# Kernel tuning notes

Hardware: AMD Instinct MI355X
Metric: run time of the kernel (lower is better)

## Reference

```python
import jax, jax.numpy as jnp
import numpy as np

B, N, G, OUT = 2, 250000, 64, 64          # batches, points per batch, grid per axis, out feat dim
NS = B * G * G * G                          # total voxel segments
EPS = 1e-5


def _bn(x, g, b, m, v):
    # BatchNorm1d in eval mode: affine with running stats
    return (x - m) * (g * jax.lax.rsqrt(v + EPS)) + b


def setup_inputs() -> dict:
    key = jax.random.key(0)
    ks = jax.random.split(key, 32)
    d = {}
    d["pt_fea"] = jax.random.normal(ks[0], (B, N, 3), jnp.float32)
    d["pt_ind"] = jax.random.randint(ks[1], (B, N, 3), 0, G)
    i = 2
    for j, dm in enumerate([3, 64, 128, 256]):
        d[f"bn{j}_g"] = jax.random.uniform(ks[i], (dm,), jnp.float32, 0.5, 1.5); i += 1
        d[f"bn{j}_b"] = jax.random.normal(ks[i], (dm,), jnp.float32) * 0.1; i += 1
        d[f"bn{j}_m"] = jax.random.normal(ks[i], (dm,), jnp.float32) * 0.1; i += 1
        d[f"bn{j}_v"] = jax.random.uniform(ks[i], (dm,), jnp.float32, 0.5, 1.5); i += 1
    for j, (fi, fo) in enumerate([(3, 64), (64, 128), (128, 256), (256, OUT)]):
        d[f"W{j}"] = jax.random.normal(ks[i], (fi, fo), jnp.float32) / np.float32(np.sqrt(fi)); i += 1
        d[f"b{j}"] = jnp.zeros((fo,), jnp.float32); i += 1
    return d


def reference(pt_fea, pt_ind,
              bn0_g, bn0_b, bn0_m, bn0_v,
              bn1_g, bn1_b, bn1_m, bn1_v,
              bn2_g, bn2_b, bn2_m, bn2_v,
              bn3_g, bn3_b, bn3_m, bn3_v,
              W0, b0, W1, b1, W2, b2, W3, b3):
    P = B * N
    x = pt_fea.reshape(P, 3)
    ind = pt_ind.reshape(P, 3)                       # (x, y, z) -> reorder to (z, y, x)
    b_idx = jnp.repeat(jnp.arange(B, dtype=ind.dtype), N)
    # linearized (batch, z, y, x) voxel id; hwl reorder as in original
    seg = ((b_idx * G + ind[:, 2]) * G + ind[:, 1]) * G + ind[:, 0]

    # PPmodel: BN -> Lin -> BN -> ReLU -> Lin -> BN -> ReLU -> Lin -> BN -> ReLU -> Lin
    h = _bn(x, bn0_g, bn0_b, bn0_m, bn0_v)
    h = jax.nn.relu(_bn(h @ W0 + b0, bn1_g, bn1_b, bn1_m, bn1_v))
    h = jax.nn.relu(_bn(h @ W1 + b1, bn2_g, bn2_b, bn2_m, bn2_v))
    h = jax.nn.relu(_bn(h @ W2 + b2, bn3_g, bn3_b, bn3_m, bn3_v))
    h = h @ W3 + b3                                   # [P, OUT]

    pooled = jax.ops.segment_max(h, seg, num_segments=NS)        # [NS, OUT]
    cnt = jax.ops.segment_sum(jnp.ones((P,), jnp.float32), seg, num_segments=NS)
    # torch_scatter.scatter_max leaves empty rows at 0
    voxel_features = jnp.where(cnt[:, None] > 0, pooled, 0.0)
    return voxel_features
```

## Files before the change

### kernel.cpp

```cpp
#include <hip/hip_runtime.h>


using bf16x8 = __attribute__((ext_vector_type(8))) short;
using f32x4  = __attribute__((ext_vector_type(4))) float;

constexpr int Bc = 2, Nc = 250000, Pc = 500000, Gc = 64, NSc = 524288;
constexpr float EPSV = 1e-5f;
constexpr int W0E = 0;
constexpr int W1E = 4096;
constexpr int W2E = 20480;
constexpr int W3E = 86016;
constexpr int CB_BYTES = 2048;

#define MFMA __builtin_amdgcn_mfma_f32_16x16x32_bf16

__device__ __forceinline__ bf16x8 mk8(unsigned a, unsigned b, unsigned c, unsigned d) {
  union { unsigned u[4]; bf16x8 v; } x;
  x.u[0] = a; x.u[1] = b; x.u[2] = c; x.u[3] = d;
  return x.v;
}

__device__ __forceinline__ void gload16(const unsigned short* src, unsigned short* dst_lds) {
  __builtin_amdgcn_global_load_lds(
      (const __attribute__((address_space(1))) unsigned int*)(const void*)src,
      (__attribute__((address_space(3))) unsigned int*)(void*)dst_lds, 16, 0, 0);
}

__device__ __forceinline__ unsigned fenc(float f) {
  unsigned b = __float_as_uint(f);
  return (b & 0x80000000u) ? ~b : (b | 0x80000000u);
}
__device__ __forceinline__ unsigned fdec(unsigned u) {
  if (u == 0u) return 0u;
  return (u & 0x80000000u) ? (u & 0x7fffffffu) : ~u;
}

__global__ void init_out_kernel(uint4* __restrict__ p, int n4) {
  int i = blockIdx.x * blockDim.x + threadIdx.x;
  const int st = gridDim.x * blockDim.x;
  const uint4 z = make_uint4(0u, 0u, 0u, 0u);
  for (; i < n4; i += st) p[i] = z;
}

__global__ void decode_out_kernel(uint4* __restrict__ p, int n4) {
  int i = blockIdx.x * blockDim.x + threadIdx.x;
  const int st = gridDim.x * blockDim.x;
  for (; i < n4; i += st) {
    uint4 u = p[i];
    u.x = fdec(u.x); u.y = fdec(u.y); u.z = fdec(u.z); u.w = fdec(u.w);
    p[i] = u;
  }
}

__global__ void prep_kernel(
    const float* __restrict__ G0, const float* __restrict__ B0, const float* __restrict__ M0, const float* __restrict__ V0,
    const float* __restrict__ G1, const float* __restrict__ B1, const float* __restrict__ M1, const float* __restrict__ V1,
    const float* __restrict__ G2, const float* __restrict__ B2, const float* __restrict__ M2, const float* __restrict__ V2,
    const float* __restrict__ G3, const float* __restrict__ B3, const float* __restrict__ M3, const float* __restrict__ V3,
    const float* __restrict__ W0, const float* __restrict__ bb0,
    const float* __restrict__ W1, const float* __restrict__ bb1,
    const float* __restrict__ W2, const float* __restrict__ bb2,
    const float* __restrict__ W3, const float* __restrict__ bb3,
    float* __restrict__ cb, unsigned short* __restrict__ wsu)
{
  const int i = blockIdx.x * 256 + threadIdx.x;
  if (i < 59392) {
    const int u = i >> 9, pos = i & 511;
    const int lane = pos >> 3, j = pos & 7;
    const int row16 = lane & 15, kin = (lane >> 4) * 8 + j;
    float v; int dstbase;
    if (u < 4) {
      const int mt = u, fo = mt * 16 + row16, k = kin;
      const float t1 = G1[fo] * rsqrtf(V1[fo] + EPSV);
      v = (k < 3) ? (G0[k] * rsqrtf(V0[k] + EPSV)) * W0[k * 64 + fo] * t1 : 0.f;
      dstbase = W0E + u * 1024;
    } else if (u < 20) {
      const int q = u - 4, mt = q >> 1, kt = q & 1;
      const int fo = mt * 16 + row16, k = kt * 32 + kin;
      v = W1[k * 128 + fo] * (G2[fo] * rsqrtf(V2[fo] + EPSV));
      dstbase = W1E + q * 1024;
    } else if (u < 84) {
      const int q = u - 20, mt = q >> 2, kt = q & 3;
      const int fo = mt * 16 + row16, k = kt * 32 + kin;
      v = W2[k * 256 + fo] * (G3[fo] * rsqrtf(V3[fo] + EPSV));
      dstbase = W2E + q * 1024;
    } else {
      const int q = u - 84, kt = q >> 2, nt = q & 3;
      const int k = kt * 32 + kin, fo = nt * 16 + row16;
      v = W3[k * 64 + fo];
      dstbase = W3E + q * 1024;
    }
    const unsigned uh = __float_as_uint(v) & 0xffff0000u;
    const float lo = v - __uint_as_float(uh);
    wsu[dstbase + pos]       = (unsigned short)(uh >> 16);
    wsu[dstbase + 512 + pos] = (unsigned short)(__float_as_uint(lo) >> 16);
  } else if (i < 59904) {
    const int f = i - 59392;
    if (f < 64) {
      const int fo = f;
      const float t1 = G1[fo] * rsqrtf(V1[fo] + EPSV);
      float s = 0.f;
      for (int c = 0; c < 3; ++c) {
        const float t0 = G0[c] * rsqrtf(V0[c] + EPSV);
        s += (B0[c] - M0[c] * t0) * W0[c * 64 + fo];
      }
      cb[fo] = (bb0[fo] + s - M1[fo]) * t1 + B1[fo];
    } else if (f < 192) {
      const int fo = f - 64;
      const float t2 = G2[fo] * rsqrtf(V2[fo] + EPSV);
      cb[64 + fo] = (bb1[fo] - M2[fo]) * t2 + B2[fo];
    } else if (f < 448) {
      const int fo = f - 192;
      const float t3 = G3[fo] * rsqrtf(V3[fo] + EPSV);
      cb[192 + fo] = (bb2[fo] - M3[fo]) * t3 + B3[fo];
    } else {
      const int fo = f - 448;
      cb[448 + fo] = bb3[fo];
    }
  }
}

struct PKp { unsigned h0, h1, l0, l1; };

__device__ __forceinline__ PKp epi_relu(f32x4 d, f32x4 cbv) {
  const float e0 = fmaxf(d[0] + cbv[0], 0.f), e1 = fmaxf(d[1] + cbv[1], 0.f);
  const float e2 = fmaxf(d[2] + cbv[2], 0.f), e3 = fmaxf(d[3] + cbv[3], 0.f);
  const unsigned u0 = __float_as_uint(e0) & 0xffff0000u, u1 = __float_as_uint(e1) & 0xffff0000u;
  const unsigned u2 = __float_as_uint(e2) & 0xffff0000u, u3 = __float_as_uint(e3) & 0xffff0000u;
  PKp r;
  r.h0 = (u0 >> 16) | u1;
  r.h1 = (u2 >> 16) | u3;
  const float f0 = e0 - __uint_as_float(u0), f1 = e1 - __uint_as_float(u1);
  const float f2 = e2 - __uint_as_float(u2), f3 = e3 - __uint_as_float(u3);
  r.l0 = (__float_as_uint(f0) >> 16) | (__float_as_uint(f1) & 0xffff0000u);
  r.l1 = (__float_as_uint(f2) >> 16) | (__float_as_uint(f3) & 0xffff0000u);
  return r;
}

__device__ __forceinline__ void trans2(const PKp& A, const PKp& B, int lane,
                                       bf16x8& fh, bf16x8& fl) {
  const int idx0 = ((lane & 15) << 2) | (((lane >> 4) & 1) << 7);
  const int idx1 = idx0 + 64;
  const bool hi = lane >= 32;
  unsigned v0, v1, v2, v3;
  { unsigned a = __builtin_amdgcn_ds_bpermute(idx0, (int)A.h0), b = __builtin_amdgcn_ds_bpermute(idx0, (int)B.h0); v0 = hi ? b : a; }
  { unsigned a = __builtin_amdgcn_ds_bpermute(idx0, (int)A.h1), b = __builtin_amdgcn_ds_bpermute(idx0, (int)B.h1); v1 = hi ? b : a; }
  { unsigned a = __builtin_amdgcn_ds_bpermute(idx1, (int)A.h0), b = __builtin_amdgcn_ds_bpermute(idx1, (int)B.h0); v2 = hi ? b : a; }
  { unsigned a = __builtin_amdgcn_ds_bpermute(idx1, (int)A.h1), b = __builtin_amdgcn_ds_bpermute(idx1, (int)B.h1); v3 = hi ? b : a; }
  fh = mk8(v0, v1, v2, v3);
  { unsigned a = __builtin_amdgcn_ds_bpermute(idx0, (int)A.l0), b = __builtin_amdgcn_ds_bpermute(idx0, (int)B.l0); v0 = hi ? b : a; }
  { unsigned a = __builtin_amdgcn_ds_bpermute(idx0, (int)A.l1), b = __builtin_amdgcn_ds_bpermute(idx0, (int)B.l1); v1 = hi ? b : a; }
  { unsigned a = __builtin_amdgcn_ds_bpermute(idx1, (int)A.l0), b = __builtin_amdgcn_ds_bpermute(idx1, (int)B.l0); v2 = hi ? b : a; }
  { unsigned a = __builtin_amdgcn_ds_bpermute(idx1, (int)A.l1), b = __builtin_amdgcn_ds_bpermute(idx1, (int)B.l1); v3 = hi ? b : a; }
  fl = mk8(v0, v1, v2, v3);
}

__global__ __launch_bounds__(512, 2)
void mlp_mfma(const float* __restrict__ pt_fea, const int* __restrict__ pt_ind,
              const unsigned short* __restrict__ wsu, const float* __restrict__ cb,
              unsigned* __restrict__ out)
{
  __shared__ __align__(16) unsigned short lds[49152];

  const int tid = threadIdx.x, lane = tid & 63, wv = tid >> 6;
  const int g = lane >> 4, c16 = lane & 15;
  const int pw = (blockIdx.x * 8 + wv) * 32;

  #pragma unroll
  for (int c = 0; c < 4; ++c) {
    const int ch = wv * 4 + c;
    gload16(wsu + W1E + ch * 512 + lane * 8, &lds[ch * 512]);
  }
  #pragma unroll
  for (int c = 0; c < 8; ++c) {
    const int ch = wv * 8 + c;
    gload16(wsu + W2E + ch * 512 + lane * 8, &lds[16384 + ch * 512]);
  }

  bf16x8 b0h[2], b0l[2];
  #pragma unroll
  for (int nt = 0; nt < 2; ++nt) {
    const int p = pw + nt * 16 + c16;
    float x = 0.f, y = 0.f, z = 0.f;
    if (p < Pc) { x = pt_fea[p * 3]; y = pt_fea[p * 3 + 1]; z = pt_fea[p * 3 + 2]; }
    const unsigned ux = __float_as_uint(x) & 0xffff0000u;
    const unsigned uy = __float_as_uint(y) & 0xffff0000u;
    const unsigned uz = __float_as_uint(z) & 0xffff0000u;
    const float lx = x - __uint_as_float(ux), ly = y - __uint_as_float(uy), lz = z - __uint_as_float(uz);
    const unsigned ph0 = (ux >> 16) | uy, ph1 = (uz >> 16);
    const unsigned pl0 = (__float_as_uint(lx) >> 16) | (__float_as_uint(ly) & 0xffff0000u);
    const unsigned pl1 = (__float_as_uint(lz) >> 16);
    const bool g0ok = (g == 0);
    b0h[nt] = mk8(g0ok ? ph0 : 0u, g0ok ? ph1 : 0u, 0u, 0u);
    b0l[nt] = mk8(g0ok ? pl0 : 0u, g0ok ? pl1 : 0u, 0u, 0u);
  }

  bf16x8 B1h[2][2], B1l[2][2];
  #pragma unroll
  for (int K = 0; K < 2; ++K) {
    PKp pk[2][2];
    #pragma unroll
    for (int e = 0; e < 2; ++e) {
      const int mt = 2 * K + e;
      const bf16x8 wh = *(const bf16x8*)(wsu + W0E + mt * 1024 + lane * 8);
      const bf16x8 wl = *(const bf16x8*)(wsu + W0E + mt * 1024 + 512 + lane * 8);
      const f32x4 cbv = *(const f32x4*)(cb + mt * 16 + g * 4);
      #pragma unroll
      for (int nt = 0; nt < 2; ++nt) {
        f32x4 acc = {0.f, 0.f, 0.f, 0.f};
        acc = MFMA(wh, b0h[nt], acc, 0, 0, 0);
        acc = MFMA(wh, b0l[nt], acc, 0, 0, 0);
        acc = MFMA(wl, b0h[nt], acc, 0, 0, 0);
        pk[e][nt] = epi_relu(acc, cbv);
      }
    }
    #pragma unroll
    for (int nt = 0; nt < 2; ++nt) trans2(pk[0][nt], pk[1][nt], lane, B1h[K][nt], B1l[K][nt]);
  }

  __syncthreads();

  bf16x8 B2h[4][2], B2l[4][2];
  #pragma unroll
  for (int K = 0; K < 4; ++K) {
    PKp pk[2][2];
    #pragma unroll
    for (int e = 0; e < 2; ++e) {
      const int mt = 2 * K + e;
      bf16x8 w[2][2];
      #pragma unroll
      for (int kt = 0; kt < 2; ++kt) {
        w[kt][0] = *(const bf16x8*)&lds[(mt * 2 + kt) * 1024 + lane * 8];
        w[kt][1] = *(const bf16x8*)&lds[(mt * 2 + kt) * 1024 + 512 + lane * 8];
      }
      const f32x4 cbv = *(const f32x4*)(cb + 64 + mt * 16 + g * 4);
      #pragma unroll
      for (int nt = 0; nt < 2; ++nt) {
        f32x4 acc = {0.f, 0.f, 0.f, 0.f};
        #pragma unroll
        for (int kt = 0; kt < 2; ++kt) {
          acc = MFMA(w[kt][0], B1h[kt][nt], acc, 0, 0, 0);
          acc = MFMA(w[kt][0], B1l[kt][nt], acc, 0, 0, 0);
          acc = MFMA(w[kt][1], B1h[kt][nt], acc, 0, 0, 0);
        }
        pk[e][nt] = epi_relu(acc, cbv);
      }
    }
    #pragma unroll
    for (int nt = 0; nt < 2; ++nt) trans2(pk[0][nt], pk[1][nt], lane, B2h[K][nt], B2l[K][nt]);
  }

  f32x4 acc3[2][4];
  #pragma unroll
  for (int pm = 0; pm < 2; ++pm)
    #pragma unroll
    for (int n3 = 0; n3 < 4; ++n3) acc3[pm][n3] = (f32x4){0.f, 0.f, 0.f, 0.f};

  float c3v[4];
  #pragma unroll
  for (int n3 = 0; n3 < 4; ++n3) c3v[n3] = cb[448 + n3 * 16 + c16];

  #pragma unroll 1
  for (int half = 0; half < 2; ++half) {
    if (half == 1) {
      __syncthreads();
      #pragma unroll
      for (int c = 0; c < 8; ++c) {
        const int ch = wv * 8 + c;
        gload16(wsu + W2E + 32768 + ch * 512 + lane * 8, &lds[16384 + ch * 512]);
      }
      __syncthreads();
    }
    #pragma unroll 1
    for (int Kl = 0; Kl < 4; ++Kl) {
      const int K = half * 4 + Kl;
      PKp pk[2][2];
      #pragma unroll
      for (int e = 0; e < 2; ++e) {
        const int mtl = 2 * Kl + e;
        const int mt = half * 8 + mtl;
        bf16x8 w[4][2];
        #pragma unroll
        for (int kt = 0; kt < 4; ++kt) {
          w[kt][0] = *(const bf16x8*)&lds[16384 + (mtl * 4 + kt) * 1024 + lane * 8];
          w[kt][1] = *(const bf16x8*)&lds[16384 + (mtl * 4 + kt) * 1024 + 512 + lane * 8];
        }
        const f32x4 cbv = *(const f32x4*)(cb + 192 + mt * 16 + g * 4);
        #pragma unroll
        for (int nt = 0; nt < 2; ++nt) {
          f32x4 acc = {0.f, 0.f, 0.f, 0.f};
          #pragma unroll
          for (int kt = 0; kt < 4; ++kt) {
            acc = MFMA(w[kt][0], B2h[kt][nt], acc, 0, 0, 0);
            acc = MFMA(w[kt][0], B2l[kt][nt], acc, 0, 0, 0);
            acc = MFMA(w[kt][1], B2h[kt][nt], acc, 0, 0, 0);
          }
          pk[e][nt] = epi_relu(acc, cbv);
        }
      }
      bf16x8 w3[4][2];
      #pragma unroll
      for (int n3 = 0; n3 < 4; ++n3) {
        w3[n3][0] = *(const bf16x8*)(wsu + W3E + (K * 4 + n3) * 1024 + lane * 8);
        w3[n3][1] = *(const bf16x8*)(wsu + W3E + (K * 4 + n3) * 1024 + 512 + lane * 8);
      }
      #pragma unroll
      for (int nt = 0; nt < 2; ++nt) {
        bf16x8 a3h, a3l;
        trans2(pk[0][nt], pk[1][nt], lane, a3h, a3l);
        #pragma unroll
        for (int n3 = 0; n3 < 4; ++n3) {
          acc3[nt][n3] = MFMA(a3h, w3[n3][0], acc3[nt][n3], 0, 0, 0);
          acc3[nt][n3] = MFMA(a3l, w3[n3][0], acc3[nt][n3], 0, 0, 0);
          acc3[nt][n3] = MFMA(a3h, w3[n3][1], acc3[nt][n3], 0, 0, 0);
        }
      }
    }
  }

  #pragma unroll
  for (int pm = 0; pm < 2; ++pm) {
    #pragma unroll
    for (int j = 0; j < 4; ++j) {
      const int p = pw + pm * 16 + g * 4 + j;
      if (p < Pc) {
        const int ix = pt_ind[p * 3], iy = pt_ind[p * 3 + 1], iz = pt_ind[p * 3 + 2];
        const int b = (p >= Nc) ? 1 : 0;
        const unsigned seg = ((unsigned)(b * Gc + iz) * Gc + iy) * Gc + ix;
        unsigned* op = out + (size_t)seg * 64 + c16;
        #pragma unroll
        for (int n3 = 0; n3 < 4; ++n3) {
          atomicMax(op + n3 * 16, fenc(acc3[pm][n3][j] + c3v[n3]));
        }
      }
    }
  }
}

extern "C" void kernel_launch(void* const* d_in, const int* in_sizes, int n_in,
                              void* d_out, int out_size, void* d_ws, size_t ws_size,
                              hipStream_t stream) {
  const float* pt_fea = (const float*)d_in[0];
  const int*   pt_ind = (const int*)d_in[1];

  float* cb = (float*)d_ws;
  unsigned short* wsu = (unsigned short*)((char*)d_ws + CB_BYTES);

  hipLaunchKernelGGL(prep_kernel, dim3(234), dim3(256), 0, stream,
                     (const float*)d_in[2],  (const float*)d_in[3],  (const float*)d_in[4],  (const float*)d_in[5],
                     (const float*)d_in[6],  (const float*)d_in[7],  (const float*)d_in[8],  (const float*)d_in[9],
                     (const float*)d_in[10], (const float*)d_in[11], (const float*)d_in[12], (const float*)d_in[13],
                     (const float*)d_in[14], (const float*)d_in[15], (const float*)d_in[16], (const float*)d_in[17],
                     (const float*)d_in[18], (const float*)d_in[19], (const float*)d_in[20], (const float*)d_in[21],
                     (const float*)d_in[22], (const float*)d_in[23], (const float*)d_in[24], (const float*)d_in[25],
                     cb, wsu);

  const int n4 = NSc * 64 / 4;
  hipLaunchKernelGGL(init_out_kernel, dim3(4096), dim3(256), 0, stream, (uint4*)d_out, n4);

  const int nblk = (Pc / 32 + 7) / 8;
  hipLaunchKernelGGL(mlp_mfma, dim3(nblk), dim3(512), 0, stream,
                     pt_fea, pt_ind, wsu, cb, (unsigned*)d_out);

  hipLaunchKernelGGL(decode_out_kernel, dim3(4096), dim3(256), 0, stream, (uint4*)d_out, n4);
}
```

Baseline: 469.2 us.

## Shrink LDS, raise occupancy, fold bias into MFMA accumulator, merge init into prep

Layer-1 weights are now read directly from global/L1 rather than staged in LDS, which cuts LDS use from 96KB to 64KB per block and lets launch bounds ask for 4 blocks per CU. The bias is used as the starting value of each MFMA accumulator instead of being added in the epilogue. The output-zeroing kernel is merged into the weight-prep kernel as extra blocks, saving one launch. The risk is register spilling at the higher occupancy target and more global-load latency for the W1 fragments.

```diff
diff --git a/kernel.cpp b/kernel.cpp
--- a/kernel.cpp
+++ b/kernel.cpp
@@ -35,13 +35,6 @@
   return (u & 0x80000000u) ? (u & 0x7fffffffu) : ~u;
 }
 
-__global__ void init_out_kernel(uint4* __restrict__ p, int n4) {
-  int i = blockIdx.x * blockDim.x + threadIdx.x;
-  const int st = gridDim.x * blockDim.x;
-  const uint4 z = make_uint4(0u, 0u, 0u, 0u);
-  for (; i < n4; i += st) p[i] = z;
-}
-
 __global__ void decode_out_kernel(uint4* __restrict__ p, int n4) {
   int i = blockIdx.x * blockDim.x + threadIdx.x;
   const int st = gridDim.x * blockDim.x;
@@ -52,7 +45,7 @@
   }
 }
 
-__global__ void prep_kernel(
+__global__ void prep_init_kernel(
     const float* __restrict__ G0, const float* __restrict__ B0, const float* __restrict__ M0, const float* __restrict__ V0,
     const float* __restrict__ G1, const float* __restrict__ B1, const float* __restrict__ M1, const float* __restrict__ V1,
     const float* __restrict__ G2, const float* __restrict__ B2, const float* __restrict__ M2, const float* __restrict__ V2,
@@ -61,8 +54,16 @@
     const float* __restrict__ W1, const float* __restrict__ bb1,
     const float* __restrict__ W2, const float* __restrict__ bb2,
     const float* __restrict__ W3, const float* __restrict__ bb3,
-    float* __restrict__ cb, unsigned short* __restrict__ wsu)
+    float* __restrict__ cb, unsigned short* __restrict__ wsu,
+    uint4* __restrict__ outp, int n4)
 {
+  if (blockIdx.x >= 234) {
+    int i = (blockIdx.x - 234) * blockDim.x + threadIdx.x;
+    const int st = (gridDim.x - 234) * blockDim.x;
+    const uint4 z = make_uint4(0u, 0u, 0u, 0u);
+    for (; i < n4; i += st) outp[i] = z;
+    return;
+  }
   const int i = blockIdx.x * 256 + threadIdx.x;
   if (i < 59392) {
     const int u = i >> 9, pos = i & 511;
@@ -122,9 +123,9 @@
 
 struct PKp { unsigned h0, h1, l0, l1; };
 
-__device__ __forceinline__ PKp epi_relu(f32x4 d, f32x4 cbv) {
-  const float e0 = fmaxf(d[0] + cbv[0], 0.f), e1 = fmaxf(d[1] + cbv[1], 0.f);
-  const float e2 = fmaxf(d[2] + cbv[2], 0.f), e3 = fmaxf(d[3] + cbv[3], 0.f);
+__device__ __forceinline__ PKp epi_relu(f32x4 d) {
+  const float e0 = fmaxf(d[0], 0.f), e1 = fmaxf(d[1], 0.f);
+  const float e2 = fmaxf(d[2], 0.f), e3 = fmaxf(d[3], 0.f);
   const unsigned u0 = __float_as_uint(e0) & 0xffff0000u, u1 = __float_as_uint(e1) & 0xffff0000u;
   const unsigned u2 = __float_as_uint(e2) & 0xffff0000u, u3 = __float_as_uint(e3) & 0xffff0000u;
   PKp r;
@@ -155,26 +156,21 @@
   fl = mk8(v0, v1, v2, v3);
 }
 
-__global__ __launch_bounds__(512, 2)
+__global__ __launch_bounds__(512, 4)
 void mlp_mfma(const float* __restrict__ pt_fea, const int* __restrict__ pt_ind,
               const unsigned short* __restrict__ wsu, const float* __restrict__ cb,
               unsigned* __restrict__ out)
 {
-  __shared__ __align__(16) unsigned short lds[49152];
+  __shared__ __align__(16) unsigned short lds[32768];
 
   const int tid = threadIdx.x, lane = tid & 63, wv = tid >> 6;
   const int g = lane >> 4, c16 = lane & 15;
   const int pw = (blockIdx.x * 8 + wv) * 32;
 
   #pragma unroll
-  for (int c = 0; c < 4; ++c) {
-    const int ch = wv * 4 + c;
-    gload16(wsu + W1E + ch * 512 + lane * 8, &lds[ch * 512]);
-  }
-  #pragma unroll
   for (int c = 0; c < 8; ++c) {
     const int ch = wv * 8 + c;
-    gload16(wsu + W2E + ch * 512 + lane * 8, &lds[16384 + ch * 512]);
+    gload16(wsu + W2E + ch * 512 + lane * 8, &lds[ch * 512]);
   }
 
   bf16x8 b0h[2], b0l[2];
@@ -207,18 +203,16 @@
       const f32x4 cbv = *(const f32x4*)(cb + mt * 16 + g * 4);
       #pragma unroll
       for (int nt = 0; nt < 2; ++nt) {
-        f32x4 acc = {0.f, 0.f, 0.f, 0.f};
+        f32x4 acc = cbv;
         acc = MFMA(wh, b0h[nt], acc, 0, 0, 0);
         acc = MFMA(wh, b0l[nt], acc, 0, 0, 0);
         acc = MFMA(wl, b0h[nt], acc, 0, 0, 0);
-        pk[e][nt] = epi_relu(acc, cbv);
+        pk[e][nt] = epi_relu(acc);
       }
     }
     #pragma unroll
     for (int nt = 0; nt < 2; ++nt) trans2(pk[0][nt], pk[1][nt], lane, B1h[K][nt], B1l[K][nt]);
   }
-
-  __syncthreads();
 
   bf16x8 B2h[4][2], B2l[4][2];
   #pragma unroll
@@ -230,35 +224,39 @@
       bf16x8 w[2][2];
       #pragma unroll
       for (int kt = 0; kt < 2; ++kt) {
-        w[kt][0] = *(const bf16x8*)&lds[(mt * 2 + kt) * 1024 + lane * 8];
-        w[kt][1] = *(const bf16x8*)&lds[(mt * 2 + kt) * 1024 + 512 + lane * 8];
+        const unsigned short* wp = wsu + W1E + (mt * 2 + kt) * 1024 + lane * 8;
+        w[kt][0] = *(const bf16x8*)wp;
+        w[kt][1] = *(const bf16x8*)(wp + 512);
       }
       const f32x4 cbv = *(const f32x4*)(cb + 64 + mt * 16 + g * 4);
       #pragma unroll
       for (int nt = 0; nt < 2; ++nt) {
-        f32x4 acc = {0.f, 0.f, 0.f, 0.f};
+        f32x4 acc = cbv;
         #pragma unroll
         for (int kt = 0; kt < 2; ++kt) {
           acc = MFMA(w[kt][0], B1h[kt][nt], acc, 0, 0, 0);
           acc = MFMA(w[kt][0], B1l[kt][nt], acc, 0, 0, 0);
           acc = MFMA(w[kt][1], B1h[kt][nt], acc, 0, 0, 0);
         }
-        pk[e][nt] = epi_relu(acc, cbv);
+        pk[e][nt] = epi_relu(acc);
       }
     }
     #pragma unroll
     for (int nt = 0; nt < 2; ++nt) trans2(pk[0][nt], pk[1][nt], lane, B2h[K][nt], B2l[K][nt]);
   }
 
+  __syncthreads();
+
+  float c3v[4];
+  #pragma unroll
+  for (int n3 = 0; n3 < 4; ++n3) c3v[n3] = cb[448 + n3 * 16 + c16];
+
   f32x4 acc3[2][4];
   #pragma unroll
   for (int pm = 0; pm < 2; ++pm)
     #pragma unroll
-    for (int n3 = 0; n3 < 4; ++n3) acc3[pm][n3] = (f32x4){0.f, 0.f, 0.f, 0.f};
-
-  float c3v[4];
-  #pragma unroll
-  for (int n3 = 0; n3 < 4; ++n3) c3v[n3] = cb[448 + n3 * 16 + c16];
+    for (int n3 = 0; n3 < 4; ++n3)
+      acc3[pm][n3] = (f32x4){c3v[n3], c3v[n3], c3v[n3], c3v[n3]};
 
   #pragma unroll 1
   for (int half = 0; half < 2; ++half) {
@@ -267,7 +265,7 @@
       #pragma unroll
       for (int c = 0; c < 8; ++c) {
         const int ch = wv * 8 + c;
-        gload16(wsu + W2E + 32768 + ch * 512 + lane * 8, &lds[16384 + ch * 512]);
+        gload16(wsu + W2E + 32768 + ch * 512 + lane * 8, &lds[ch * 512]);
       }
       __syncthreads();
     }
@@ -282,20 +280,20 @@
         bf16x8 w[4][2];
         #pragma unroll
         for (int kt = 0; kt < 4; ++kt) {
-          w[kt][0] = *(const bf16x8*)&lds[16384 + (mtl * 4 + kt) * 1024 + lane * 8];
-          w[kt][1] = *(const bf16x8*)&lds[16384 + (mtl * 4 + kt) * 1024 + 512 + lane * 8];
+          w[kt][0] = *(const bf16x8*)&lds[(mtl * 4 + kt) * 1024 + lane * 8];
+          w[kt][1] = *(const bf16x8*)&lds[(mtl * 4 + kt) * 1024 + 512 + lane * 8];
         }
         const f32x4 cbv = *(const f32x4*)(cb + 192 + mt * 16 + g * 4);
         #pragma unroll
         for (int nt = 0; nt < 2; ++nt) {
-          f32x4 acc = {0.f, 0.f, 0.f, 0.f};
+          f32x4 acc = cbv;
           #pragma unroll
           for (int kt = 0; kt < 4; ++kt) {
             acc = MFMA(w[kt][0], B2h[kt][nt], acc, 0, 0, 0);
             acc = MFMA(w[kt][0], B2l[kt][nt], acc, 0, 0, 0);
             acc = MFMA(w[kt][1], B2h[kt][nt], acc, 0, 0, 0);
           }
-          pk[e][nt] = epi_relu(acc, cbv);
+          pk[e][nt] = epi_relu(acc);
         }
       }
       bf16x8 w3[4][2];
@@ -330,7 +328,7 @@
         unsigned* op = out + (size_t)seg * 64 + c16;
         #pragma unroll
         for (int n3 = 0; n3 < 4; ++n3) {
-          atomicMax(op + n3 * 16, fenc(acc3[pm][n3][j] + c3v[n3]));
+          atomicMax(op + n3 * 16, fenc(acc3[pm][n3][j]));
         }
       }
     }
@@ -346,17 +344,15 @@
   float* cb = (float*)d_ws;
   unsigned short* wsu = (unsigned short*)((char*)d_ws + CB_BYTES);
 
-  hipLaunchKernelGGL(prep_kernel, dim3(234), dim3(256), 0, stream,
+  const int n4 = NSc * 64 / 4;
+  hipLaunchKernelGGL(prep_init_kernel, dim3(234 + 4096), dim3(256), 0, stream,
                      (const float*)d_in[2],  (const float*)d_in[3],  (const float*)d_in[4],  (const float*)d_in[5],
                      (const float*)d_in[6],  (const float*)d_in[7],  (const float*)d_in[8],  (const float*)d_in[9],
                      (const float*)d_in[10], (const float*)d_in[11], (const float*)d_in[12], (const float*)d_in[13],
                      (const float*)d_in[14], (const float*)d_in[15], (const float*)d_in[16], (const float*)d_in[17],
                      (const float*)d_in[18], (const float*)d_in[19], (const float*)d_in[20], (const float*)d_in[21],
                      (const float*)d_in[22], (const float*)d_in[23], (const float*)d_in[24], (const float*)d_in[25],
-                     cb, wsu);
-
-  const int n4 = NSc * 64 / 4;
-  hipLaunchKernelGGL(init_out_kernel, dim3(4096), dim3(256), 0, stream, (uint4*)d_out, n4);
+                     cb, wsu, (uint4*)d_out, n4);
 
   const int nblk = (Pc / 32 + 7) / 8;
   hipLaunchKernelGGL(mlp_mfma, dim3(nblk), dim3(512), 0, stream,
```

Result: slower. 523.5 us (+11.6%).
